# Kernel tuning notes

Hardware: AMD Instinct MI355X
Metric: run time of the kernel (lower is better)

## Reference

```python
import jax, jax.numpy as jnp
import numpy as np

D_MODEL = 1024
NHEAD = 16
HEAD_DIM = D_MODEL // NHEAD
MAX_LEN = 4096
ROPE_BASE = 500.0


def _rope_tables(L, dim):
    inv_freq = 1.0 / (ROPE_BASE ** (jnp.arange(0, dim, 2, dtype=jnp.float32) / dim))
    t = jnp.arange(L, dtype=jnp.float32)
    freqs = jnp.einsum('i,j->ij', t, inv_freq)  # [L, dim/2]
    emb = jnp.concatenate([freqs, freqs], axis=-1)  # [L, dim]
    return jnp.cos(emb), jnp.sin(emb)


def _rotate_half(x):
    x1, x2 = jnp.split(x, 2, axis=-1)
    return jnp.concatenate([-x2, x1], axis=-1)


def _apply_rope(x, cos, sin):
    return x * cos + _rotate_half(x) * sin


def setup_inputs() -> dict:
    key = jax.random.key(0)
    ks = jax.random.split(key, 6)
    B, L = 4, 2048
    bound_qkv = 1.0 / np.sqrt(D_MODEL)
    x = jax.random.normal(ks[0], (B, L, D_MODEL), dtype=jnp.float32)
    key_padding_mask = jnp.zeros((B, L), dtype=bool)
    W_qkv = jax.random.uniform(ks[1], (3 * D_MODEL, D_MODEL), jnp.float32, -bound_qkv, bound_qkv)
    b_qkv = jax.random.uniform(ks[2], (3 * D_MODEL,), jnp.float32, -bound_qkv, bound_qkv)
    W_out = jax.random.uniform(ks[3], (D_MODEL, D_MODEL), jnp.float32, -bound_qkv, bound_qkv)
    b_out = jax.random.uniform(ks[4], (D_MODEL,), jnp.float32, -bound_qkv, bound_qkv)
    return {"x": x, "key_padding_mask": key_padding_mask,
            "W_qkv": W_qkv, "b_qkv": b_qkv, "W_out": W_out, "b_out": b_out}


def reference(x, key_padding_mask, W_qkv, b_qkv, W_out, b_out):
    B, L, D = x.shape
    H, hd = NHEAD, HEAD_DIM
    qkv = x @ W_qkv.T + b_qkv  # [B, L, 3D]
    q, k, v = jnp.split(qkv, 3, axis=-1)
    # [B, H, L, hd]
    q = q.reshape(B, L, H, hd).transpose(0, 2, 1, 3)
    k = k.reshape(B, L, H, hd).transpose(0, 2, 1, 3)
    v = v.reshape(B, L, H, hd).transpose(0, 2, 1, 3)
    cos, sin = _rope_tables(L, hd)  # [L, hd]
    q = _apply_rope(q, cos, sin)
    k = _apply_rope(k, cos, sin)
    scores = jnp.einsum('bhqd,bhkd->bhqk', q, k) / jnp.sqrt(jnp.float32(hd))
    mask = key_padding_mask[:, None, None, :]  # [B,1,1,L]
    scores = jnp.where(mask, -jnp.inf, scores)
    attn = jax.nn.softmax(scores, axis=-1)
    out = jnp.einsum('bhqk,bhkd->bhqd', attn, v)
    out = out.transpose(0, 2, 1, 3).reshape(B, L, D)
    return out @ W_out.T + b_out
```

## Files before the change

kernel.cpp:

```cpp
#include <hip/hip_runtime.h>
#include <stdint.h>

typedef __attribute__((ext_vector_type(8))) __bf16 bf16x8;
typedef __attribute__((ext_vector_type(4))) short short4v;
typedef __attribute__((ext_vector_type(4))) float f32x4;

#if __has_builtin(__builtin_amdgcn_exp2f)
#define EXP2(x) __builtin_amdgcn_exp2f(x)
#else
#define EXP2(x) exp2f(x)
#endif

__device__ __forceinline__ short f2bf(float f) {
  union { float f; uint32_t u; } v; v.f = f;
  uint32_t r = (v.u + 0x7fffu + ((v.u >> 16) & 1u)) >> 16;
  return (short)(uint16_t)r;
}

__device__ __forceinline__ uint32_t pk2bf(float a, float b) {
  union { __bf16 h; uint16_t u; } x, y;
  x.h = (__bf16)a; y.h = (__bf16)b;
  return (uint32_t)x.u | ((uint32_t)y.u << 16);
}

__device__ __forceinline__ void gl2lds16(const void* g, const void* lds) {
  __builtin_amdgcn_global_load_lds(
      (const __attribute__((address_space(1))) void*)(uintptr_t)g,
      (__attribute__((address_space(3))) void*)(uint32_t)(uintptr_t)lds,
      16, 0, 0);
}

__device__ __forceinline__ bf16x8 frag8(const short* p) {
  return *(const bf16x8*)(const void*)p;
}

__global__ void convert3_k(const float* __restrict__ s0, short* __restrict__ d0, int n0,
                           const float* __restrict__ s1, short* __restrict__ d1, int n1,
                           const float* __restrict__ s2, short* __restrict__ d2, int n2) {
  int i = blockIdx.x * blockDim.x + threadIdx.x;
  int t0 = n0 >> 2, t1 = t0 + (n1 >> 2), t2 = t1 + (n2 >> 2);
  const float* s; short* d; int off;
  if (i < t0) { s = s0; d = d0; off = i; }
  else if (i < t1) { s = s1; d = d1; off = i - t0; }
  else if (i < t2) { s = s2; d = d2; off = i - t1; }
  else return;
  float4 v = ((const float4*)s)[off];
  short4v o;
  o.x = f2bf(v.x); o.y = f2bf(v.y); o.z = f2bf(v.z); o.w = f2bf(v.w);
  *(short4v*)(d + off * 4) = o;
}

__global__ void rope_tab_k(float* __restrict__ cosT, float* __restrict__ sinT,
                           const unsigned char* __restrict__ mask, float* __restrict__ maskf) {
  int i = blockIdx.x * blockDim.x + threadIdx.x;
  int pos = i >> 5, j = i & 31;
  float invf = exp2f(-(float)j * (8.965784284662087f / 32.0f));
  float ang = (float)pos * invf;
  float s, c;
  sincosf(ang, &s, &c);
  cosT[i] = c; sinT[i] = s;
  if (i < 8192) maskf[i] = mask[i] ? -1e30f : 0.0f;
}

template <int EPI>
__global__
void gemm_bt_k(const short* __restrict__ A, const short* __restrict__ Bm,
               const float* __restrict__ bias, int N, int K,
               float* __restrict__ Cout,
               const float* __restrict__ cosT, const float* __restrict__ sinT,
               short* __restrict__ Qb, short* __restrict__ Kb, short* __restrict__ Vt) {
  __shared__ short As[128 * 32];
  __shared__ short Bs[128 * 32];
  const int tid = threadIdx.x;
  const int lane = tid & 63;
  const int w = tid >> 6;
  const int g = lane >> 4, l15 = lane & 15;
  const int wm = (w >> 1) * 64, wn = (w & 1) * 64;
  const int bm = blockIdx.x, bn = blockIdx.y;

  const int rseg = lane >> 2;
  const int cofs = ((lane & 3) ^ ((lane >> 3) & 3)) * 8;
  const int sA0 = w, sA1 = w + 4;
  const int arow0 = (bm * 128 + sA0 * 16 + rseg) * K;
  const int arow1 = (bm * 128 + sA1 * 16 + rseg) * K;
  const int brow0 = (bn * 128 + sA0 * 16 + rseg) * K;
  const int brow1 = (bn * 128 + sA1 * 16 + rseg) * K;

  const int rsw = (l15 >> 1) & 3;

  f32x4 acc[4][4];
#pragma unroll
  for (int i = 0; i < 4; i++)
#pragma unroll
    for (int j = 0; j < 4; j++) acc[i][j] = f32x4{0.f, 0.f, 0.f, 0.f};

  for (int k0 = 0; k0 < K; k0 += 32) {
    gl2lds16(A + arow0 + k0 + cofs, &As[sA0 * 512]);
    gl2lds16(A + arow1 + k0 + cofs, &As[sA1 * 512]);
    gl2lds16(Bm + brow0 + k0 + cofs, &Bs[sA0 * 512]);
    gl2lds16(Bm + brow1 + k0 + cofs, &Bs[sA1 * 512]);
    __syncthreads();
    bf16x8 af[4], bf[4];
#pragma unroll
    for (int im = 0; im < 4; im++) af[im] = frag8(&As[(wm + im * 16 + l15) * 32 + (g ^ rsw) * 8]);
#pragma unroll
    for (int jn = 0; jn < 4; jn++) bf[jn] = frag8(&Bs[(wn + jn * 16 + l15) * 32 + (g ^ rsw) * 8]);
#pragma unroll
    for (int im = 0; im < 4; im++)
#pragma unroll
      for (int jn = 0; jn < 4; jn++)
        acc[im][jn] = __builtin_amdgcn_mfma_f32_16x16x32_bf16(af[im], bf[jn], acc[im][jn], 0, 0, 0);
    __syncthreads();
  }

  const int row0 = bm * 128 + wm + g * 4;
  const int col0 = bn * 128 + wn;

  if (EPI == 0) {
#pragma unroll
    for (int jn = 0; jn < 4; jn++) {
      float bb = bias[col0 + jn * 16 + l15];
#pragma unroll
      for (int im = 0; im < 4; im++)
#pragma unroll
        for (int r = 0; r < 4; r++) {
          int row = row0 + im * 16 + r;
          Cout[row * N + col0 + jn * 16 + l15] = acc[im][jn][r] + bb;
        }
    }
  } else {
#pragma unroll
    for (int jn = 0; jn < 4; jn++) {
      float bb = bias[col0 + jn * 16 + l15];
#pragma unroll
      for (int im = 0; im < 4; im++)
#pragma unroll
        for (int r = 0; r < 4; r++) acc[im][jn][r] += bb;
    }
    const int sector = col0 >> 10;
    const int h = (col0 & 1023) >> 6;
    if (sector == 2) {
#pragma unroll
      for (int jn = 0; jn < 4; jn++) {
        int d = jn * 16 + l15;
#pragma unroll
        for (int im = 0; im < 4; im++) {
          int row = row0 + im * 16;
          int b = row >> 11, pos = row & 2047;
          union { uint32_t u[2]; short4v s4; } pw;
          pw.u[0] = pk2bf(acc[im][jn][0], acc[im][jn][1]);
          pw.u[1] = pk2bf(acc[im][jn][2], acc[im][jn][3]);
          *(short4v*)&Vt[((b * 16 + h) * 64 + d) * 2048 + pos] = pw.s4;
        }
      }
    } else {
      short* dst = (sector == 0) ? Qb : Kb;
      const float scl = (sector == 0) ? 0.18033688011112042f : 1.0f;
#pragma unroll
      for (int jn = 0; jn < 4; jn++) {
        int d = jn * 16 + l15;
        int j = d & 31;
#pragma unroll
        for (int im = 0; im < 4; im++)
#pragma unroll
          for (int r = 0; r < 4; r++) {
            int row = row0 + im * 16 + r;
            int b = row >> 11, pos = row & 2047;
            float c = cosT[pos * 32 + j];
            float s = sinT[pos * 32 + j];
            float xv = acc[im][jn][r];
            float xp = acc[im][jn ^ 2][r];
            float rot = (jn < 2) ? -xp : xp;
            dst[((b * 16 + h) * 2048 + pos) * 64 + d] = f2bf((xv * c + rot * s) * scl);
          }
      }
    }
  }
}

__global__ __launch_bounds__(256, 4)
void attn_k(const short* __restrict__ Qb, const short* __restrict__ Kb,
            const short* __restrict__ Vt, const float* __restrict__ maskf,
            short* __restrict__ attn) {
  __shared__ short Ks[64 * 64];
  __shared__ short Vs[64 * 64];
  __shared__ short Ps[4][32 * 64];
  const int tid = threadIdx.x, lane = tid & 63, w = tid >> 6;
  const int g = lane >> 4, l15 = lane & 15;
  const int sw = l15 & 7;
  const int qt = blockIdx.x, bh = blockIdx.y;
  const int b = bh >> 4, h = bh & 15;

  bf16x8 aq[2][2];
#pragma unroll
  for (int qi = 0; qi < 2; qi++)
#pragma unroll
    for (int kc = 0; kc < 2; kc++) {
      int q = qt * 128 + w * 32 + qi * 16 + l15;
      aq[qi][kc] = *(const bf16x8*)(const void*)(Qb + (bh * 2048 + q) * 64 + kc * 32 + g * 8);
    }
  bf16x8 aone;
#pragma unroll
  for (int i = 0; i < 8; i++) aone[i] = (__bf16)1.0f;

  f32x4 o[4][2];
#pragma unroll
  for (int jd = 0; jd < 4; jd++)
#pragma unroll
    for (int qi = 0; qi < 2; qi++) o[jd][qi] = f32x4{0.f, 0.f, 0.f, 0.f};
  f32x4 lacc[2] = {f32x4{0.f, 0.f, 0.f, 0.f}, f32x4{0.f, 0.f, 0.f, 0.f}};

  const float* mfp = maskf + b * 2048;
  const int r8 = lane >> 3;
  const int cst = (lane & 7) ^ r8;

  for (int kt = 0; kt < 32; kt++) {
    const int kbase = kt * 64;
#pragma unroll
    for (int t = 0; t < 4; t++) {
      int s = w * 4 + t;
      if (s < 8) {
        gl2lds16(Kb + (bh * 2048 + kbase + s * 8 + r8) * 64 + cst * 8, &Ks[s * 512]);
      } else {
        gl2lds16(Vt + (bh * 64 + (s - 8) * 8 + r8) * 2048 + kbase + cst * 8, &Vs[(s - 8) * 512]);
      }
    }
    __syncthreads();

    f32x4 sv[4][2];
#pragma unroll
    for (int kvt = 0; kvt < 4; kvt++) {
      f32x4 mf = *(const f32x4*)(mfp + kbase + kvt * 16 + g * 4);
      sv[kvt][0] = mf; sv[kvt][1] = mf;
    }
#pragma unroll
    for (int kvt = 0; kvt < 4; kvt++)
#pragma unroll
      for (int kc = 0; kc < 2; kc++) {
        bf16x8 ak = frag8(&Ks[(kvt * 16 + l15) * 64 + ((kc * 4 + g) ^ sw) * 8]);
        sv[kvt][0] = __builtin_amdgcn_mfma_f32_16x16x32_bf16(ak, aq[0][kc], sv[kvt][0], 0, 0, 0);
        sv[kvt][1] = __builtin_amdgcn_mfma_f32_16x16x32_bf16(ak, aq[1][kc], sv[kvt][1], 0, 0, 0);
      }

#pragma unroll
    for (int qi = 0; qi < 2; qi++)
#pragma unroll
      for (int kvt = 0; kvt < 4; kvt++) {
        union { uint32_t u[2]; short4v s4; } pw;
        pw.u[0] = pk2bf(EXP2(sv[kvt][qi][0]), EXP2(sv[kvt][qi][1]));
        pw.u[1] = pk2bf(EXP2(sv[kvt][qi][2]), EXP2(sv[kvt][qi][3]));
        *(short4v*)&Ps[w][(qi * 16 + l15) * 64 + ((2 * kvt + (g >> 1)) ^ sw) * 8 + (g & 1) * 4] = pw.s4;
      }

#pragma unroll
    for (int kc = 0; kc < 2; kc++) {
      bf16x8 av[4];
#pragma unroll
      for (int jd = 0; jd < 4; jd++)
        av[jd] = frag8(&Vs[(jd * 16 + l15) * 64 + ((kc * 4 + g) ^ sw) * 8]);
#pragma unroll
      for (int qi = 0; qi < 2; qi++) {
        bf16x8 bp = frag8(&Ps[w][(qi * 16 + l15) * 64 + ((kc * 4 + g) ^ sw) * 8]);
#pragma unroll
        for (int jd = 0; jd < 4; jd++)
          o[jd][qi] = __builtin_amdgcn_mfma_f32_16x16x32_bf16(av[jd], bp, o[jd][qi], 0, 0, 0);
        lacc[qi] = __builtin_amdgcn_mfma_f32_16x16x32_bf16(aone, bp, lacc[qi], 0, 0, 0);
      }
    }
    __syncthreads();
  }

#pragma unroll
  for (int qi = 0; qi < 2; qi++) {
    float inv = 1.0f / lacc[qi][0];
    int q = qt * 128 + w * 32 + qi * 16 + l15;
#pragma unroll
    for (int jd = 0; jd < 4; jd++) {
      union { uint32_t u[2]; short4v s4; } pw;
      pw.u[0] = pk2bf(o[jd][qi][0] * inv, o[jd][qi][1] * inv);
      pw.u[1] = pk2bf(o[jd][qi][2] * inv, o[jd][qi][3] * inv);
      *(short4v*)&attn[(b * 2048 + q) * 1024 + h * 64 + jd * 16 + g * 4] = pw.s4;
    }
  }
}

extern "C" void kernel_launch(void* const* d_in, const int* in_sizes, int n_in,
                              void* d_out, int out_size, void* d_ws, size_t ws_size,
                              hipStream_t stream) {
  const float* x = (const float*)d_in[0];
  const unsigned char* mask = (const unsigned char*)d_in[1];
  const float* W_qkv = (const float*)d_in[2];
  const float* b_qkv = (const float*)d_in[3];
  const float* W_out = (const float*)d_in[4];
  const float* b_out = (const float*)d_in[5];
  float* out = (float*)d_out;

  char* ws = (char*)d_ws;
  short* xb    = (short*)(ws + 0);
  short* wqkvb = (short*)(ws + 16777216);
  short* woutb = (short*)(ws + 23068672);
  float* cosT  = (float*)(ws + 25165824);
  float* sinT  = (float*)(ws + 25427968);
  short* Qb    = (short*)(ws + 25690112);
  short* Kb    = (short*)(ws + 42467328);
  short* Vtb   = (short*)(ws + 59244544);
  short* attnb = (short*)(ws + 76021760);
  float* maskf = (float*)(ws + 92798976);

  convert3_k<<<12288, 256, 0, stream>>>(x, xb, 8388608, W_qkv, wqkvb, 3145728, W_out, woutb, 1048576);
  rope_tab_k<<<256, 256, 0, stream>>>(cosT, sinT, mask, maskf);
  gemm_bt_k<1><<<dim3(64, 24), 256, 0, stream>>>(xb, wqkvb, b_qkv, 3072, 1024,
                                                 nullptr, cosT, sinT, Qb, Kb, Vtb);
  attn_k<<<dim3(16, 64), 256, 0, stream>>>(Qb, Kb, Vtb, maskf, attnb);
  gemm_bt_k<0><<<dim3(64, 8), 256, 0, stream>>>(attnb, woutb, b_out, 1024, 1024,
                                                out, nullptr, nullptr, nullptr, nullptr, nullptr);
}
```

Measured before the change: 304.1 us.

## Double-buffer LDS tiles in GEMM and attention kernels with one barrier per step

Both the projection GEMM and the attention kernel now keep two LDS buffers for their K/V (or A/B) tiles. Each step prefetches the next tile while computing on the current one, with a single barrier per iteration instead of two. The aim is to hide global-to-LDS load latency behind MFMA work. In exchange LDS use doubles, so the attention kernel's launch bound drops from 4 to 3 blocks per CU and the GEMM gets a launch bound of 3, which lowers occupancy.

```diff
diff --git a/kernel.cpp b/kernel.cpp
--- a/kernel.cpp
+++ b/kernel.cpp
@@ -63,14 +63,14 @@
 }
 
 template <int EPI>
-__global__
+__global__ __launch_bounds__(256, 3)
 void gemm_bt_k(const short* __restrict__ A, const short* __restrict__ Bm,
                const float* __restrict__ bias, int N, int K,
                float* __restrict__ Cout,
                const float* __restrict__ cosT, const float* __restrict__ sinT,
                short* __restrict__ Qb, short* __restrict__ Kb, short* __restrict__ Vt) {
-  __shared__ short As[128 * 32];
-  __shared__ short Bs[128 * 32];
+  __shared__ short As[2][128 * 32];
+  __shared__ short Bs[2][128 * 32];
   const int tid = threadIdx.x;
   const int lane = tid & 63;
   const int w = tid >> 6;
@@ -94,23 +94,32 @@
 #pragma unroll
     for (int j = 0; j < 4; j++) acc[i][j] = f32x4{0.f, 0.f, 0.f, 0.f};
 
-  for (int k0 = 0; k0 < K; k0 += 32) {
-    gl2lds16(A + arow0 + k0 + cofs, &As[sA0 * 512]);
-    gl2lds16(A + arow1 + k0 + cofs, &As[sA1 * 512]);
-    gl2lds16(Bm + brow0 + k0 + cofs, &Bs[sA0 * 512]);
-    gl2lds16(Bm + brow1 + k0 + cofs, &Bs[sA1 * 512]);
+  gl2lds16(A + arow0 + cofs, &As[0][sA0 * 512]);
+  gl2lds16(A + arow1 + cofs, &As[0][sA1 * 512]);
+  gl2lds16(Bm + brow0 + cofs, &Bs[0][sA0 * 512]);
+  gl2lds16(Bm + brow1 + cofs, &Bs[0][sA1 * 512]);
+
+  int cur = 0;
+  for (int k0 = 0; k0 < K; k0 += 32, cur ^= 1) {
     __syncthreads();
+    int nxt = cur ^ 1;
+    int k1 = k0 + 32;
+    if (k1 < K) {
+      gl2lds16(A + arow0 + k1 + cofs, &As[nxt][sA0 * 512]);
+      gl2lds16(A + arow1 + k1 + cofs, &As[nxt][sA1 * 512]);
+      gl2lds16(Bm + brow0 + k1 + cofs, &Bs[nxt][sA0 * 512]);
+      gl2lds16(Bm + brow1 + k1 + cofs, &Bs[nxt][sA1 * 512]);
+    }
     bf16x8 af[4], bf[4];
 #pragma unroll
-    for (int im = 0; im < 4; im++) af[im] = frag8(&As[(wm + im * 16 + l15) * 32 + (g ^ rsw) * 8]);
-#pragma unroll
-    for (int jn = 0; jn < 4; jn++) bf[jn] = frag8(&Bs[(wn + jn * 16 + l15) * 32 + (g ^ rsw) * 8]);
+    for (int im = 0; im < 4; im++) af[im] = frag8(&As[cur][(wm + im * 16 + l15) * 32 + (g ^ rsw) * 8]);
+#pragma unroll
+    for (int jn = 0; jn < 4; jn++) bf[jn] = frag8(&Bs[cur][(wn + jn * 16 + l15) * 32 + (g ^ rsw) * 8]);
 #pragma unroll
     for (int im = 0; im < 4; im++)
 #pragma unroll
       for (int jn = 0; jn < 4; jn++)
         acc[im][jn] = __builtin_amdgcn_mfma_f32_16x16x32_bf16(af[im], bf[jn], acc[im][jn], 0, 0, 0);
-    __syncthreads();
   }
 
   const int row0 = bm * 128 + wm + g * 4;
@@ -178,12 +187,12 @@
   }
 }
 
-__global__ __launch_bounds__(256, 4)
+__global__ __launch_bounds__(256, 3)
 void attn_k(const short* __restrict__ Qb, const short* __restrict__ Kb,
             const short* __restrict__ Vt, const float* __restrict__ maskf,
             short* __restrict__ attn) {
-  __shared__ short Ks[64 * 64];
-  __shared__ short Vs[64 * 64];
+  __shared__ short Ks[2][64 * 64];
+  __shared__ short Vs[2][64 * 64];
   __shared__ short Ps[4][32 * 64];
   const int tid = threadIdx.x, lane = tid & 63, w = tid >> 6;
   const int g = lane >> 4, l15 = lane & 15;
@@ -213,19 +222,29 @@
   const float* mfp = maskf + b * 2048;
   const int r8 = lane >> 3;
   const int cst = (lane & 7) ^ r8;
-
-  for (int kt = 0; kt < 32; kt++) {
+  const int t0s = w * 4;
+
+#pragma unroll
+  for (int t = 0; t < 4; t++) {
+    int s = t0s + t;
+    if (s < 8) gl2lds16(Kb + (bh * 2048 + s * 8 + r8) * 64 + cst * 8, &Ks[0][s * 512]);
+    else       gl2lds16(Vt + (bh * 64 + (s - 8) * 8 + r8) * 2048 + cst * 8, &Vs[0][(s - 8) * 512]);
+  }
+
+  int cur = 0;
+  for (int kt = 0; kt < 32; kt++, cur ^= 1) {
     const int kbase = kt * 64;
-#pragma unroll
-    for (int t = 0; t < 4; t++) {
-      int s = w * 4 + t;
-      if (s < 8) {
-        gl2lds16(Kb + (bh * 2048 + kbase + s * 8 + r8) * 64 + cst * 8, &Ks[s * 512]);
-      } else {
-        gl2lds16(Vt + (bh * 64 + (s - 8) * 8 + r8) * 2048 + kbase + cst * 8, &Vs[(s - 8) * 512]);
-      }
-    }
     __syncthreads();
+    int nxt = cur ^ 1;
+    if (kt + 1 < 32) {
+      const int nb = kbase + 64;
+#pragma unroll
+      for (int t = 0; t < 4; t++) {
+        int s = t0s + t;
+        if (s < 8) gl2lds16(Kb + (bh * 2048 + nb + s * 8 + r8) * 64 + cst * 8, &Ks[nxt][s * 512]);
+        else       gl2lds16(Vt + (bh * 64 + (s - 8) * 8 + r8) * 2048 + nb + cst * 8, &Vs[nxt][(s - 8) * 512]);
+      }
+    }
 
     f32x4 sv[4][2];
 #pragma unroll
@@ -237,7 +256,7 @@
     for (int kvt = 0; kvt < 4; kvt++)
 #pragma unroll
       for (int kc = 0; kc < 2; kc++) {
-        bf16x8 ak = frag8(&Ks[(kvt * 16 + l15) * 64 + ((kc * 4 + g) ^ sw) * 8]);
+        bf16x8 ak = frag8(&Ks[cur][(kvt * 16 + l15) * 64 + ((kc * 4 + g) ^ sw) * 8]);
         sv[kvt][0] = __builtin_amdgcn_mfma_f32_16x16x32_bf16(ak, aq[0][kc], sv[kvt][0], 0, 0, 0);
         sv[kvt][1] = __builtin_amdgcn_mfma_f32_16x16x32_bf16(ak, aq[1][kc], sv[kvt][1], 0, 0, 0);
       }
@@ -257,7 +276,7 @@
       bf16x8 av[4];
 #pragma unroll
       for (int jd = 0; jd < 4; jd++)
-        av[jd] = frag8(&Vs[(jd * 16 + l15) * 64 + ((kc * 4 + g) ^ sw) * 8]);
+        av[jd] = frag8(&Vs[cur][(jd * 16 + l15) * 64 + ((kc * 4 + g) ^ sw) * 8]);
 #pragma unroll
       for (int qi = 0; qi < 2; qi++) {
         bf16x8 bp = frag8(&Ps[w][(qi * 16 + l15) * 64 + ((kc * 4 + g) ^ sw) * 8]);
@@ -267,7 +286,6 @@
         lacc[qi] = __builtin_amdgcn_mfma_f32_16x16x32_bf16(aone, bp, lacc[qi], 0, 0, 0);
       }
     }
-    __syncthreads();
   }
 
 #pragma unroll
```

Result: no change. 304.3 us (+0.1%).
